# Performance work log

Measured on AMD Instinct MI355X. Metric: run time of the kernel, lower is better.

Reference implementation:

```python
import jax, jax.numpy as jnp
import numpy as np

BETA = 0.25


def setup_inputs() -> dict:
    key = jax.random.key(0)
    k1, k2, k3, k4 = jax.random.split(key, 4)
    B, D, T, H, W = 2, 256, 8, 32, 32
    K = 8192
    z = jax.random.normal(k1, (B, D, T, H, W), dtype=jnp.float32)
    # nn.init.normal_(embedding.weight, mean=0, std=emb_dim ** -0.5)
    emb_w = jax.random.normal(k2, (K, D), dtype=jnp.float32) * (D ** -0.5)
    # torch Linear default init ~ U(-1/sqrt(in), 1/sqrt(in)); scaled normal is fine for a reference
    w1 = jax.random.normal(k3, (D, D), dtype=jnp.float32) * (D ** -0.5)
    w2 = jax.random.normal(k4, (D, D), dtype=jnp.float32) * (D ** -0.5)
    return {"z": z, "emb_w": emb_w, "w1": w1, "w2": w2}


def reference(z, emb_w, w1, w2):
    B, D, T, H, W = z.shape
    K = emb_w.shape[0]
    # permute to channels-last and flatten: [B,T,H,W,D] -> [N,D]
    z_cl = jnp.transpose(z, (0, 2, 3, 4, 1))
    z_flat = z_cl.reshape(-1, D)
    N = z_flat.shape[0]
    # simvq: Linear -> GELU (exact) -> Linear, both bias-free
    quant_codebook = jax.nn.gelu(emb_w @ w1.T, approximate=False) @ w2.T  # [K, D]
    # pairwise squared L2 distances [N, K]
    d = (
        jnp.sum(z_flat ** 2, axis=1, keepdims=True)
        + jnp.sum(quant_codebook ** 2, axis=1)
        - 2.0 * (z_flat @ quant_codebook.T)
    )
    mean_distance = jnp.mean(d)
    idx = jnp.argmin(d, axis=1)  # [N]
    # gather == one-hot @ codebook
    z_q_flat = quant_codebook[idx]  # [N, D]
    z_q = z_q_flat.reshape(z_cl.shape)
    # VQ loss with stop-gradients
    loss = jnp.mean((jax.lax.stop_gradient(z_q) - z_cl) ** 2) + BETA * jnp.mean(
        (z_q - jax.lax.stop_gradient(z_cl)) ** 2
    )
    # straight-through estimator
    z_q = z_cl + jax.lax.stop_gradient(z_q - z_cl)
    # perplexity from code usage histogram (== mean of one-hot encodings)
    counts = jnp.zeros((K,), dtype=jnp.float32).at[idx].add(1.0)
    e_mean = counts / N
    perplexity = jnp.exp(-jnp.sum(e_mean * jnp.log(e_mean + 1e-10)))
    # back to channels-first [B, D, T, H, W]
    z_q = jnp.transpose(z_q, (0, 4, 1, 2, 3))
    return z_q, loss, perplexity, mean_distance
```

## Files before the change

### kernel.cpp

```cpp
#include <hip/hip_runtime.h>
#include <math.h>

#define BATCH 2
#define DIM   256
#define THW   8192
#define NTOK  16384
#define KCB   8192
#define OUTQ  4194304
#define CAP   2000000
#define SCAP  5600

typedef short short8 __attribute__((ext_vector_type(8)));
typedef float f32x4 __attribute__((ext_vector_type(4)));

__device__ __forceinline__ unsigned short f2bf_rn(float v) {
    unsigned u = __float_as_uint(v);
    unsigned r = u + 0x7FFFu + ((u >> 16) & 1u);
    return (unsigned short)(r >> 16);
}
__device__ __forceinline__ float bf2f(unsigned short b) {
    return __uint_as_float((unsigned)b << 16);
}
__device__ __forceinline__ void gl2lds16(const unsigned short* g, unsigned short* l) {
    __builtin_amdgcn_global_load_lds(
        (const __attribute__((address_space(1))) void*)g,
        (__attribute__((address_space(3))) void*)l, 16, 0, 0);
}

__global__ void k_splitW(const float* __restrict__ w1, const float* __restrict__ w2,
                         unsigned short* __restrict__ W1s, unsigned short* __restrict__ W2s,
                         int* __restrict__ counts,
                         unsigned* __restrict__ tileMaxC, unsigned* __restrict__ tileMaxCl,
                         float* __restrict__ accums,
                         float* __restrict__ partialZ, float* __restrict__ partialC) {
    int bid = blockIdx.x;
    int t = threadIdx.x;
    if (bid < 32) {
        counts[bid * 256 + t] = 0;
    } else if (bid == 32) {
        if (t < 64) { tileMaxC[t] = 0u; tileMaxCl[t] = 0u; }
        if (t >= 64 && t < 72) accums[t - 64] = 0.f;
    } else if (bid == 33) {
        partialZ[t] = 0.f;
    } else if (bid == 34) {
        partialC[t] = 0.f;
    }
    int row = bid & 255;
    const float* src = (bid >> 8) ? w2 : w1;
    unsigned short* dst = ((bid >> 8) ? W2s : W1s) + (size_t)row * 768;
    float v = src[row * 256 + t];
    unsigned short hb = f2bf_rn(v);
    unsigned short lb = f2bf_rn(v - bf2f(hb));
    dst[t] = hb;
    dst[256 + t] = hb;
    dst[512 + t] = lb;
}

__global__ void k_buildA(const float* __restrict__ z,
                         unsigned short* __restrict__ Ahi,
                         unsigned short* __restrict__ Alo,
                         float* __restrict__ zsq,
                         float* __restrict__ sA, float* __restrict__ sB,
                         float* __restrict__ partialZ,
                         unsigned long long* __restrict__ packed,
                         unsigned long long* __restrict__ packed2) {
    __shared__ ushort2 tile[64][65];
    __shared__ float zacc[64];
    __shared__ float lacc[64];
    __shared__ float pz[256];
    int t = threadIdx.x;
    int n0 = blockIdx.x * 64;
    int b = n0 >> 13;
    int thw0 = n0 & 8191;
    if (t < 64) {
        zacc[t] = 0.f; lacc[t] = 0.f;
        packed[n0 + t] = ~0ull;
        packed2[n0 + t] = ~0ull;
    }
    pz[t] = 0.f;
    __syncthreads();
    int nn_r = t & 63, dg = t >> 6;
    float a1 = 0.f, a2 = 0.f;
    for (int dc = 0; dc < 256; dc += 64) {
        for (int r = 0; r < 16; ++r) {
            int dd = r * 4 + dg;
            float v = z[((size_t)(b * 256 + dc + dd)) * 8192 + thw0 + nn_r];
            unsigned short hb = f2bf_rn(v);
            float hf = bf2f(hb);
            unsigned short lb = f2bf_rn(v - hf);
            float lf = bf2f(lb);
            tile[dd][nn_r] = make_ushort2(hb, lb);
            a1 += v * v;
            a2 += lf * lf;
        }
        __syncthreads();
        int kk = t & 63, ng = t >> 6;
        float dimsum = 0.f;
        for (int i2 = 0; i2 < 16; ++i2) {
            int nn = ng + i2 * 4;
            ushort2 hl = tile[kk][nn];
            size_t base = (size_t)(n0 + nn) * 256;
            Ahi[base + dc + kk] = hl.x;
            Alo[base + dc + kk] = hl.y;
            dimsum += bf2f(hl.x) + bf2f(hl.y);
        }
        atomicAdd(&pz[dc + kk], dimsum);
        __syncthreads();
    }
    atomicAdd(&zacc[nn_r], a1);
    atomicAdd(&lacc[nn_r], a2);
    __syncthreads();
    if (t < 64) {
        zsq[n0 + t] = zacc[t];
        sA[n0 + t] = 2.1f * sqrtf(lacc[t]);
        sB[n0 + t] = 2.1f * sqrtf(zacc[t]);
    }
    atomicAdd(&partialZ[t], pz[t]);
}

__global__ void k_buildE(const float* __restrict__ emb, unsigned short* __restrict__ E) {
    int t = threadIdx.x;
    int row = blockIdx.x * 4 + (t >> 6);
    int e4 = (t & 63) * 4;
    float4 v = *(const float4*)&emb[(size_t)row * 256 + e4];
    ushort4 hi, lo;
    hi.x = f2bf_rn(v.x); lo.x = f2bf_rn(v.x - bf2f(hi.x));
    hi.y = f2bf_rn(v.y); lo.y = f2bf_rn(v.y - bf2f(hi.y));
    hi.z = f2bf_rn(v.z); lo.z = f2bf_rn(v.z - bf2f(hi.z));
    hi.w = f2bf_rn(v.w); lo.w = f2bf_rn(v.w - bf2f(hi.w));
    size_t base = (size_t)row * 768;
    *(ushort4*)&E[base + e4] = hi;
    *(ushort4*)&E[base + 256 + e4] = lo;
    *(ushort4*)&E[base + 512 + e4] = hi;
}

template <int GELU>
__global__ __launch_bounds__(256) void k_mlp(const unsigned short* __restrict__ A,
                                             const unsigned short* __restrict__ B,
                                             unsigned short* __restrict__ Hs,
                                             float* __restrict__ C_t) {
    __shared__ __align__(16) char smem[32768];
    unsigned short* Asm = (unsigned short*)smem;
    unsigned short* Bsm = (unsigned short*)(smem + 16384);

    int t = threadIdx.x;
    int lane = t & 63;
    int w = t >> 6;
    int wm = w >> 1, wn = w & 1;
    int m0 = blockIdx.y * 128;
    int n0 = blockIdx.x * 128;

    int rA = w * 8 + (lane >> 3);
    int ch_l = lane & 7;
    int ch_g = ch_l ^ (lane >> 3);
    const unsigned short* gA = A + (size_t)(m0 + rA) * 768 + ch_g * 8;
    const unsigned short* gB = B + (size_t)(n0 + rA) * 768 + ch_g * 8;
    unsigned short* lA = &Asm[rA * 64 + ch_l * 8];
    unsigned short* lB = &Bsm[rA * 64 + ch_l * 8];

    f32x4 acc[4][4];
#pragma unroll
    for (int i = 0; i < 4; ++i)
#pragma unroll
        for (int j = 0; j < 4; ++j)
            acc[i][j] = f32x4{0.f, 0.f, 0.f, 0.f};

#pragma unroll
    for (int i = 0; i < 4; ++i) {
        gl2lds16(gA + (size_t)(32 * i) * 768, lA + 32 * i * 64);
        gl2lds16(gB + (size_t)(32 * i) * 768, lB + 32 * i * 64);
    }
    __syncthreads();

    int l15 = lane & 15;
    int quad = lane >> 4;
    int sw = l15 & 7;
    for (int kc = 0; kc < 12; ++kc) {
#pragma unroll
        for (int kk = 0; kk < 2; ++kk) {
            short8 a[4], b[4];
#pragma unroll
            for (int i = 0; i < 4; ++i)
                a[i] = *(const short8*)&Asm[(wm * 64 + i * 16 + l15) * 64 +
                                            (((kk * 4 + quad) ^ sw) * 8)];
#pragma unroll
            for (int j = 0; j < 4; ++j)
                b[j] = *(const short8*)&Bsm[(wn * 64 + j * 16 + l15) * 64 +
                                            (((kk * 4 + quad) ^ sw) * 8)];
#pragma unroll
            for (int i = 0; i < 4; ++i)
#pragma unroll
                for (int j = 0; j < 4; ++j)
                    acc[i][j] = __builtin_amdgcn_mfma_f32_16x16x32_bf16(a[i], b[j], acc[i][j], 0, 0, 0);
        }
        __syncthreads();
        if (kc < 11) {
            int ko = (kc + 1) * 64;
#pragma unroll
            for (int i = 0; i < 4; ++i) {
                gl2lds16(gA + (size_t)(32 * i) * 768 + ko, lA + 32 * i * 64);
                gl2lds16(gB + (size_t)(32 * i) * 768 + ko, lB + 32 * i * 64);
            }
            __syncthreads();
        }
    }

#pragma unroll
    for (int i = 0; i < 4; ++i) {
#pragma unroll
        for (int reg = 0; reg < 4; ++reg) {
            int mrow = m0 + wm * 64 + i * 16 + quad * 4 + reg;
#pragma unroll
            for (int j = 0; j < 4; ++j) {
                int ncol = n0 + wn * 64 + j * 16 + l15;
                float h = acc[i][j][reg];
                if (GELU) {
                    float g = 0.5f * h * (1.f + erff(h * 0.70710678118654752f));
                    unsigned short hb = f2bf_rn(g);
                    unsigned short lb = f2bf_rn(g - bf2f(hb));
                    size_t base = (size_t)mrow * 768;
                    Hs[base + ncol] = hb;
                    Hs[base + 256 + ncol] = lb;
                    Hs[base + 512 + ncol] = hb;
                } else {
                    C_t[(size_t)mrow * 8192 + ncol] = h;
                }
            }
        }
    }
}

__global__ void k_buildB(const float* __restrict__ C_t,
                         unsigned short* __restrict__ Bhi,
                         unsigned short* __restrict__ Blo,
                         float* __restrict__ csq,
                         float* __restrict__ sC, float* __restrict__ sCl,
                         unsigned* __restrict__ tileMaxC, unsigned* __restrict__ tileMaxCl,
                         float* __restrict__ accums, float* __restrict__ partialC) {
    __shared__ ushort2 tile[64][65];
    __shared__ float kacc[64];
    __shared__ float lacc[64];
    __shared__ float pc[256];
    int t = threadIdx.x;
    int k0 = blockIdx.x * 64;
    if (t < 64) { kacc[t] = 0.f; lacc[t] = 0.f; }
    pc[t] = 0.f;
    __syncthreads();
    int nn_r = t & 63, dg = t >> 6;
    float a1 = 0.f, a2 = 0.f;
    for (int dc = 0; dc < 256; dc += 64) {
        for (int r = 0; r < 16; ++r) {
            int dd = r * 4 + dg;
            float v = C_t[(size_t)(dc + dd) * KCB + k0 + nn_r];
            unsigned short hb = f2bf_rn(v);
            float hf = bf2f(hb);
            unsigned short lb = f2bf_rn(v - hf);
            float lf = bf2f(lb);
            tile[dd][nn_r] = make_ushort2(hb, lb);
            a1 += v * v;
            a2 += lf * lf;
        }
        __syncthreads();
        int kk = t & 63, ng = t >> 6;
        float dimsum = 0.f;
        for (int i2 = 0; i2 < 16; ++i2) {
            int nn = ng + i2 * 4;
            ushort2 hl = tile[kk][nn];
            size_t base = (size_t)(k0 + nn) * 256;
            Bhi[base + dc + kk] = hl.x;
            Blo[base + dc + kk] = hl.y;
            dimsum += bf2f(hl.x) + bf2f(hl.y);
        }
        atomicAdd(&pc[dc + kk], dimsum);
        __syncthreads();
    }
    atomicAdd(&kacc[nn_r], a1);
    atomicAdd(&lacc[nn_r], a2);
    __syncthreads();
    if (t < 64) {
        float c2 = kacc[t], l2 = lacc[t];
        float sc = sqrtf(c2), sl = sqrtf(l2);
        csq[k0 + t] = c2;
        sC[k0 + t] = sc;
        sCl[k0 + t] = sl;
        int tl = blockIdx.x >> 1;
        atomicMax(&tileMaxC[tl], __float_as_uint(sc));
        atomicMax(&tileMaxCl[tl], __float_as_uint(sl));
        atomicMax((unsigned*)&accums[3], __float_as_uint(c2));
        atomicMax((unsigned*)&accums[4], __float_as_uint(l2));
    }
    atomicAdd(&partialC[t], pc[t]);
}

__global__ __launch_bounds__(512, 2) void k_dist_hi(const unsigned short* __restrict__ A,
                                                    const unsigned short* __restrict__ B,
                                                    const float* __restrict__ zsq,
                                                    const float* __restrict__ csq,
                                                    const float* __restrict__ sA,
                                                    const float* __restrict__ sB,
                                                    const unsigned* __restrict__ tileMaxC,
                                                    const unsigned* __restrict__ tileMaxCl,
                                                    unsigned long long* __restrict__ packed,
                                                    float* __restrict__ accums,
                                                    unsigned long long* __restrict__ cand) {
    __shared__ __align__(16) char smem[131072];
    float* sbd     = (float*)smem;
    float* gprev_s = (float*)(smem + 2048);
    float* thr     = (float*)(smem + 3072);
    unsigned* scnt  = (unsigned*)(smem + 4096);
    unsigned* sbase = (unsigned*)(smem + 4100);
    unsigned long long* scand = (unsigned long long*)(smem + 4112);

    int t = threadIdx.x;
    int lane = t & 63;
    int w = t >> 6;
    int wm = w >> 1, wn = w & 1;
    int m0 = blockIdx.x * 256;
    int n0 = blockIdx.y * 256;

    int rA0 = w * 8 + (lane >> 3);
    int ch_l = lane & 7;
    int ch_g = ch_l ^ (lane >> 3);
    const unsigned short* gA = A + (size_t)(m0 + rA0) * 256 + ch_g * 8;
    const unsigned short* gB = B + (size_t)(n0 + rA0) * 256 + ch_g * 8;
    unsigned short* smemU = (unsigned short*)smem;
    unsigned short* lA = smemU + rA0 * 64 + ch_l * 8;
    unsigned short* lB = smemU + 16384 + rA0 * 64 + ch_l * 8;

    int l15 = lane & 15;
    int quad = lane >> 4;
    int sw = l15 & 7;

    float M1 = sqrtf(accums[3]);
    float M2 = sqrtf(accums[4]);
    float msC  = fmaxf(__uint_as_float(tileMaxC[2 * blockIdx.y]),
                       __uint_as_float(tileMaxC[2 * blockIdx.y + 1]));
    float msCl = fmaxf(__uint_as_float(tileMaxCl[2 * blockIdx.y]),
                       __uint_as_float(tileMaxCl[2 * blockIdx.y + 1]));
    float cv[8];
    int cols[8];
#pragma unroll
    for (int j = 0; j < 8; ++j) {
        int cloc = wn * 128 + j * 16 + l15;
        cols[j] = n0 + cloc;
        cv[j] = csq[cols[j]];
    }

    f32x4 acc[4][8];
#pragma unroll
    for (int i = 0; i < 4; ++i)
#pragma unroll
        for (int j = 0; j < 8; ++j)
            acc[i][j] = f32x4{0.f, 0.f, 0.f, 0.f};

#define STAGE(B_, KO)                                                       \
    {                                                                       \
        int off_ = (B_) * 32768;                                            \
        _Pragma("unroll")                                                   \
        for (int i_ = 0; i_ < 4; ++i_)                                      \
            gl2lds16(gA + (size_t)(64 * i_) * 256 + (KO),                   \
                     lA + off_ + 64 * i_ * 64);                             \
        _Pragma("unroll")                                                   \
        for (int i_ = 0; i_ < 4; ++i_)                                      \
            gl2lds16(gB + (size_t)(64 * i_) * 256 + (KO),                   \
                     lB + off_ + 64 * i_ * 64);                             \
    }

    STAGE(0, 0)
    __syncthreads();

    int cur = 0;
    for (int kc = 0; kc < 4; ++kc) {
        if (kc < 3) STAGE(cur ^ 1, (kc + 1) * 64)
        const unsigned short* Ar = smemU + cur * 32768;
        const unsigned short* Br = Ar + 16384;
#pragma unroll
        for (int kk = 0; kk < 2; ++kk) {
            short8 a[4], b[8];
#pragma unroll
            for (int i = 0; i < 4; ++i)
                a[i] = *(const short8*)&Ar[(wm * 64 + i * 16 + l15) * 64 +
                                            (((kk * 4 + quad) ^ sw) * 8)];
#pragma unroll
            for (int j = 0; j < 8; ++j)
                b[j] = *(const short8*)&Br[(wn * 128 + j * 16 + l15) * 64 +
                                            (((kk * 4 + quad) ^ sw) * 8)];
#pragma unroll
            for (int i = 0; i < 4; ++i)
#pragma unroll
                for (int j = 0; j < 8; ++j)
                    acc[i][j] = __builtin_amdgcn_mfma_f32_16x16x32_bf16(a[i], b[j], acc[i][j], 0, 0, 0);
        }
        __syncthreads();
        cur ^= 1;
    }
#undef STAGE

    if (t == 0) *scnt = 0;
    if (t < 256) {
        const unsigned* hp = (const unsigned*)&packed[m0 + t];
        gprev_s[t] = __uint_as_float(__atomic_load_n(hp + 1, __ATOMIC_RELAXED));
    }
#pragma unroll
    for (int i = 0; i < 4; ++i) {
#pragma unroll
        for (int reg = 0; reg < 4; ++reg) {
            int rloc = wm * 64 + i * 16 + quad * 4 + reg;
            float zs = zsq[m0 + rloc];
            float bd = 3.4e38f;
#pragma unroll
            for (int j = 0; j < 8; ++j) {
                float d = (zs + cv[j]) - 2.0f * acc[i][j][reg];
                acc[i][j][reg] = d;
                bd = fminf(bd, d);
            }
#pragma unroll
            for (int off = 1; off < 16; off <<= 1)
                bd = fminf(bd, __shfl_xor(bd, off, 64));
            if (l15 == 0) sbd[wn * 256 + rloc] = bd;
        }
    }
    __syncthreads();
    if (t < 256) {
        float bd = fminf(sbd[t], sbd[256 + t]);
        atomicMin(&packed[m0 + t], (unsigned long long)__float_as_uint(bd) << 32);
        float g = fminf(bd, gprev_s[t]);
        thr[t] = g + 1e-3f + sA[m0 + t] * (M1 + msC) + sB[m0 + t] * (M2 + msCl);
    }
    __syncthreads();
    unsigned* cnt = (unsigned*)&accums[2];
#pragma unroll
    for (int i = 0; i < 4; ++i) {
#pragma unroll
        for (int reg = 0; reg < 4; ++reg) {
            int rloc = wm * 64 + i * 16 + quad * 4 + reg;
            float tr = thr[rloc];
            bool p[8];
            bool any = false;
#pragma unroll
            for (int j = 0; j < 8; ++j) {
                p[j] = acc[i][j][reg] <= tr;
                any |= p[j];
            }
            if (__ballot(any)) {
                unsigned rbits = (unsigned)((m0 + rloc) << 13);
#pragma unroll
                for (int j = 0; j < 8; ++j) {
                    if (p[j]) {
                        unsigned long long entry =
                            ((unsigned long long)__float_as_uint(acc[i][j][reg]) << 32) |
                            (rbits | (unsigned)cols[j]);
                        unsigned pos = atomicAdd(scnt, 1u);
                        if (pos < SCAP) scand[pos] = entry;
                        else {
                            unsigned gp2 = atomicAdd(cnt, 1u);
                            if (gp2 < CAP) cand[gp2] = entry;
                        }
                    }
                }
            }
        }
    }
    __syncthreads();
    if (t == 0) {
        unsigned m = *scnt;
        if (m > SCAP) m = SCAP;
        *scnt = m;
        *sbase = atomicAdd(cnt, m);
    }
    __syncthreads();
    {
        unsigned m = *scnt, b0 = *sbase;
        for (unsigned u = t; u < m; u += 512)
            if (b0 + u < CAP) cand[b0 + u] = scand[u];
    }
}

__global__ __launch_bounds__(256) void k_rescore(const unsigned long long* __restrict__ cand,
                                                 const unsigned short* __restrict__ Ahi,
                                                 const unsigned short* __restrict__ Alo,
                                                 const unsigned short* __restrict__ Bhi,
                                                 const unsigned short* __restrict__ Blo,
                                                 const float* __restrict__ zsq,
                                                 const float* __restrict__ csq,
                                                 const float* __restrict__ sA,
                                                 const float* __restrict__ sB,
                                                 const float* __restrict__ sC,
                                                 const float* __restrict__ sCl,
                                                 const unsigned long long* __restrict__ packed,
                                                 unsigned long long* __restrict__ packed2,
                                                 const float* __restrict__ accums) {
    __shared__ unsigned long long q[256];
    __shared__ unsigned qn;
    unsigned total = *(const unsigned*)&accums[2];
    if (total > CAP) total = CAP;
    float M1 = sqrtf(accums[3]);
    float M2 = sqrtf(accums[4]);
    int t = threadIdx.x;
    int lane = t & 63;
    int w = t >> 6;
    unsigned per = (total + gridDim.x - 1) / gridDim.x;
    unsigned e0 = blockIdx.x * per;
    unsigned e1 = e0 + per;
    if (e1 > total) e1 = total;
    for (unsigned base = e0; base < e1; base += 256) {
        if (t == 0) qn = 0;
        __syncthreads();
        unsigned e = base + (unsigned)t;
        bool pass = false;
        unsigned long long ent = 0;
        if (e < e1) {
            ent = cand[e];
            float dhi = __uint_as_float((unsigned)(ent >> 32));
            unsigned nk = (unsigned)ent;
            int n = (nk >> 13) & 16383;
            int k = nk & 8191;
            float g = __uint_as_float((unsigned)(packed[n] >> 32));
            float marg = g + 1e-3f + sA[n] * (M1 + sC[k]) + sB[n] * (M2 + sCl[k]);
            pass = (dhi <= marg);
        }
        unsigned long long mask = __ballot(pass);
        if (mask) {
            unsigned cw = (unsigned)__popcll(mask);
            unsigned wbase = 0;
            if (lane == 0) wbase = atomicAdd(&qn, cw);
            wbase = __shfl(wbase, 0, 64);
            if (pass) {
                unsigned pos = wbase +
                    (unsigned)__popcll(mask & ((1ull << lane) - 1ull));
                q[pos] = ent;
            }
        }
        __syncthreads();
        unsigned m = qn;
        for (unsigned i = (unsigned)w; i < m; i += 4) {
            unsigned long long e2 = q[i];
            unsigned nk = (unsigned)e2;
            int n = (nk >> 13) & 16383;
            int k = nk & 8191;
            ushort4 zh = *((const ushort4*)(Ahi + (size_t)n * 256) + lane);
            ushort4 zl = *((const ushort4*)(Alo + (size_t)n * 256) + lane);
            ushort4 ch = *((const ushort4*)(Bhi + (size_t)k * 256) + lane);
            ushort4 cl = *((const ushort4*)(Blo + (size_t)k * 256) + lane);
            float s = (bf2f(zh.x) + bf2f(zl.x)) * (bf2f(ch.x) + bf2f(cl.x))
                    + (bf2f(zh.y) + bf2f(zl.y)) * (bf2f(ch.y) + bf2f(cl.y))
                    + (bf2f(zh.z) + bf2f(zl.z)) * (bf2f(ch.z) + bf2f(cl.z))
                    + (bf2f(zh.w) + bf2f(zl.w)) * (bf2f(ch.w) + bf2f(cl.w));
#pragma unroll
            for (int off = 1; off < 64; off <<= 1)
                s += __shfl_xor(s, off, 64);
            if (lane == 0) {
                float dd = (zsq[n] + csq[k]) - 2.0f * s;
                unsigned long long p =
                    ((unsigned long long)__float_as_uint(dd) << 32) | (unsigned)k;
                atomicMin(&packed2[n], p);
            }
        }
        __syncthreads();
    }
}

__global__ void k_zqloss(const float* __restrict__ z, const float* __restrict__ C_t,
                         const unsigned long long* __restrict__ packed2,
                         float* __restrict__ out, float* __restrict__ loss_sum,
                         int* __restrict__ counts) {
    __shared__ float red[256];
    int bid = blockIdx.x;
    int b = bid >> 8;
    int d = bid & 255;
    int t = threadIdx.x;
    if (t < 32) {
        int kk = (int)(unsigned)packed2[bid * 32 + t] & 8191;
        atomicAdd(&counts[kk], 1);
    }
    const float* crow = C_t + (size_t)d * KCB;
    const unsigned long long* pb = packed2 + (size_t)b * THW;
    size_t base = ((size_t)(b * DIM + d)) * THW;
    float lsum = 0.f;
    for (int it = 0; it < 8; ++it) {
        int thw = it * 1024 + t * 4;
        ulonglong2 p01 = *(const ulonglong2*)&pb[thw];
        ulonglong2 p23 = *(const ulonglong2*)&pb[thw + 2];
        int i0 = (int)(unsigned)p01.x & 8191;
        int i1 = (int)(unsigned)p01.y & 8191;
        int i2 = (int)(unsigned)p23.x & 8191;
        int i3 = (int)(unsigned)p23.y & 8191;
        float4 zz = *(const float4*)&z[base + thw];
        float4 v;
        v.x = crow[i0]; v.y = crow[i1]; v.z = crow[i2]; v.w = crow[i3];
        *(float4*)&out[base + thw] = v;
        float d0 = v.x - zz.x, d1 = v.y - zz.y, d2 = v.z - zz.z, d3 = v.w - zz.w;
        lsum += d0 * d0 + d1 * d1 + d2 * d2 + d3 * d3;
    }
    red[t] = lsum;
    __syncthreads();
    for (int s = 128; s > 0; s >>= 1) {
        if (t < s) red[t] += red[t + s];
        __syncthreads();
    }
    if (t == 0) atomicAdd(loss_sum, red[0]);
}

__global__ void k_scalars(const int* __restrict__ counts,
                          const float* __restrict__ accums,
                          const float* __restrict__ zsq, const float* __restrict__ csq,
                          const float* __restrict__ partialZ,
                          const float* __restrict__ partialC,
                          float* __restrict__ out_tail) {
    __shared__ double redd[256];
    __shared__ float redf[256];
    int t = threadIdx.x;
    double szsq = 0.0, scsq = 0.0;
    for (int n = t; n < NTOK; n += 256) szsq += (double)zsq[n];
    for (int k = t; k < KCB; k += 256) scsq += (double)csq[k];
    float SZ = partialZ[t];
    float SC = partialC[t];
    double total = 8192.0 * szsq + 16384.0 * scsq - 2.0 * (double)SZ * (double)SC;
    redd[t] = total;
    float s = 0.f;
    for (int k = t; k < KCB; k += 256) {
        float e = (float)counts[k] * (1.0f / 16384.0f);
        s += e * logf(e + 1e-10f);
    }
    redf[t] = s;
    __syncthreads();
    for (int st = 128; st > 0; st >>= 1) {
        if (t < st) { redd[t] += redd[t + st]; redf[t] += redf[t + st]; }
        __syncthreads();
    }
    if (t == 0) {
        out_tail[0] = 1.25f * accums[1] / 4194304.0f;
        out_tail[1] = expf(-redf[0]);
        out_tail[2] = (float)(redd[0] / (16384.0 * 8192.0));
    }
}

extern "C" void kernel_launch(void* const* d_in, const int* in_sizes, int n_in,
                              void* d_out, int out_size, void* d_ws, size_t ws_size,
                              hipStream_t stream) {
    const float* z     = (const float*)d_in[0];
    const float* emb_w = (const float*)d_in[1];
    const float* w1    = (const float*)d_in[2];
    const float* w2    = (const float*)d_in[3];
    float* out = (float*)d_out;

    char* w = (char*)d_ws;
    unsigned short* Ahi = (unsigned short*)(w + 0);
    unsigned short* Alo = (unsigned short*)(w + 8388608);
    unsigned short* Ebf = (unsigned short*)(w + 16777216);
    unsigned short* Bhi = (unsigned short*)(w + 29360128);
    unsigned short* Blo = (unsigned short*)(w + 33554432);
    unsigned short* W1s = (unsigned short*)(w + 37748736);
    unsigned short* W2s = (unsigned short*)(w + 38141952);
    float* zsq   = (float*)(w + 38535168);
    float* sA    = (float*)(w + 38666240);
    float* sB    = (float*)(w + 38731776);
    float* csq   = (float*)(w + 38797312);
    float* sC    = (float*)(w + 38862848);
    float* sCl   = (float*)(w + 38895616);
    unsigned long long* packed  = (unsigned long long*)(w + 38928384);
    unsigned long long* packed2 = (unsigned long long*)(w + 39059456);
    int*   counts = (int*)(w + 39256064);
    float* partialZ = (float*)(w + 39288832);
    float* partialC = (float*)(w + 39550976);
    unsigned* tileMaxC  = (unsigned*)(w + 39682048);
    unsigned* tileMaxCl = (unsigned*)(w + 39682304);
    float* accums = (float*)(w + 39682560);

    float* C_t = (float*)Ebf;
    unsigned short* Hs = (unsigned short*)d_out;
    unsigned long long* cand = (unsigned long long*)d_out;

    k_splitW<<<512, 256, 0, stream>>>(w1, w2, W1s, W2s, counts,
                                      tileMaxC, tileMaxCl, accums, partialZ, partialC);
    k_buildA<<<NTOK / 64, 256, 0, stream>>>(z, Ahi, Alo, zsq, sA, sB, partialZ,
                                            packed, packed2);
    k_buildE<<<KCB / 4, 256, 0, stream>>>(emb_w, Ebf);

    k_mlp<1><<<dim3(2, KCB / 128), 256, 0, stream>>>(Ebf, W1s, Hs, nullptr);
    k_mlp<0><<<dim3(KCB / 128, 2), 256, 0, stream>>>(W2s, Hs, nullptr, C_t);

    k_buildB<<<KCB / 64, 256, 0, stream>>>(C_t, Bhi, Blo, csq, sC, sCl,
                                           tileMaxC, tileMaxCl, accums, partialC);

    k_dist_hi<<<dim3(NTOK / 256, KCB / 256), 512, 0, stream>>>(
        Ahi, Bhi, zsq, csq, sA, sB, tileMaxC, tileMaxCl, packed, accums, cand);

    k_rescore<<<1024, 256, 0, stream>>>(cand, Ahi, Alo, Bhi, Blo, zsq, csq,
                                        sA, sB, sC, sCl, packed, packed2, accums);

    k_zqloss<<<BATCH * DIM, 256, 0, stream>>>(z, C_t, packed2, out, accums + 1, counts);
    k_scalars<<<1, 256, 0, stream>>>(counts, accums, zsq, csq, partialZ, partialC, out + OUTQ);
}
```

Measured before the change: 380.3 us.

## Merge prep kernels, double-buffer MLP GEMM with 64-row tiles, widen rescore grid

Combines the three preprocessing kernels (weight split, z conversion, embedding conversion) into one launch so block roles are chosen by block index, which saves two launches. The MLP GEMM now uses 64-row M tiles to double the number of blocks, and it double-buffers LDS so the next K chunk loads while the current one is being computed. The rescore grid is doubled. The cost is larger LDS use per block and a smaller per-wave tile, which lowers MFMA reuse.

```diff
diff --git a/kernel.cpp b/kernel.cpp
--- a/kernel.cpp
+++ b/kernel.cpp
@@ -27,49 +27,63 @@
         (__attribute__((address_space(3))) void*)l, 16, 0, 0);
 }
 
-__global__ void k_splitW(const float* __restrict__ w1, const float* __restrict__ w2,
-                         unsigned short* __restrict__ W1s, unsigned short* __restrict__ W2s,
-                         int* __restrict__ counts,
-                         unsigned* __restrict__ tileMaxC, unsigned* __restrict__ tileMaxCl,
-                         float* __restrict__ accums,
-                         float* __restrict__ partialZ, float* __restrict__ partialC) {
-    int bid = blockIdx.x;
-    int t = threadIdx.x;
-    if (bid < 32) {
-        counts[bid * 256 + t] = 0;
-    } else if (bid == 32) {
-        if (t < 64) { tileMaxC[t] = 0u; tileMaxCl[t] = 0u; }
-        if (t >= 64 && t < 72) accums[t - 64] = 0.f;
-    } else if (bid == 33) {
-        partialZ[t] = 0.f;
-    } else if (bid == 34) {
-        partialC[t] = 0.f;
-    }
-    int row = bid & 255;
-    const float* src = (bid >> 8) ? w2 : w1;
-    unsigned short* dst = ((bid >> 8) ? W2s : W1s) + (size_t)row * 768;
-    float v = src[row * 256 + t];
-    unsigned short hb = f2bf_rn(v);
-    unsigned short lb = f2bf_rn(v - bf2f(hb));
-    dst[t] = hb;
-    dst[256 + t] = hb;
-    dst[512 + t] = lb;
-}
-
-__global__ void k_buildA(const float* __restrict__ z,
-                         unsigned short* __restrict__ Ahi,
-                         unsigned short* __restrict__ Alo,
-                         float* __restrict__ zsq,
-                         float* __restrict__ sA, float* __restrict__ sB,
-                         float* __restrict__ partialZ,
-                         unsigned long long* __restrict__ packed,
-                         unsigned long long* __restrict__ packed2) {
+__global__ void k_prep(const float* __restrict__ w1, const float* __restrict__ w2,
+                       unsigned short* __restrict__ W1s, unsigned short* __restrict__ W2s,
+                       int* __restrict__ counts,
+                       unsigned* __restrict__ tileMaxC, unsigned* __restrict__ tileMaxCl,
+                       float* __restrict__ accums,
+                       float* __restrict__ partialZ, float* __restrict__ partialC,
+                       const float* __restrict__ z,
+                       unsigned short* __restrict__ Ahi, unsigned short* __restrict__ Alo,
+                       float* __restrict__ zsq, float* __restrict__ sA, float* __restrict__ sB,
+                       unsigned long long* __restrict__ packed,
+                       unsigned long long* __restrict__ packed2,
+                       const float* __restrict__ emb, unsigned short* __restrict__ E) {
     __shared__ ushort2 tile[64][65];
     __shared__ float zacc[64];
     __shared__ float lacc[64];
     __shared__ float pz[256];
+    int bid = blockIdx.x;
     int t = threadIdx.x;
-    int n0 = blockIdx.x * 64;
+
+    if (bid < 512) {
+        if (bid < 32) {
+            counts[bid * 256 + t] = 0;
+        } else if (bid == 32) {
+            if (t < 64) { tileMaxC[t] = 0u; tileMaxCl[t] = 0u; }
+            if (t >= 64 && t < 72) accums[t - 64] = 0.f;
+        } else if (bid == 33) {
+            partialZ[t] = 0.f;
+        } else if (bid == 34) {
+            partialC[t] = 0.f;
+        }
+        int row = bid & 255;
+        const float* src = (bid >> 8) ? w2 : w1;
+        unsigned short* dst = ((bid >> 8) ? W2s : W1s) + (size_t)row * 768;
+        float v = src[row * 256 + t];
+        unsigned short hb = f2bf_rn(v);
+        unsigned short lb = f2bf_rn(v - bf2f(hb));
+        dst[t] = hb;
+        dst[256 + t] = hb;
+        dst[512 + t] = lb;
+        return;
+    }
+    if (bid >= 768) {
+        int row = (bid - 768) * 4 + (t >> 6);
+        int e4 = (t & 63) * 4;
+        float4 v = *(const float4*)&emb[(size_t)row * 256 + e4];
+        ushort4 hi, lo;
+        hi.x = f2bf_rn(v.x); lo.x = f2bf_rn(v.x - bf2f(hi.x));
+        hi.y = f2bf_rn(v.y); lo.y = f2bf_rn(v.y - bf2f(hi.y));
+        hi.z = f2bf_rn(v.z); lo.z = f2bf_rn(v.z - bf2f(hi.z));
+        hi.w = f2bf_rn(v.w); lo.w = f2bf_rn(v.w - bf2f(hi.w));
+        size_t base = (size_t)row * 768;
+        *(ushort4*)&E[base + e4] = hi;
+        *(ushort4*)&E[base + 256 + e4] = lo;
+        *(ushort4*)&E[base + 512 + e4] = hi;
+        return;
+    }
+    int n0 = (bid - 512) * 64;
     int b = n0 >> 13;
     int thw0 = n0 & 8191;
     if (t < 64) {
@@ -118,98 +132,85 @@
     atomicAdd(&partialZ[t], pz[t]);
 }
 
-__global__ void k_buildE(const float* __restrict__ emb, unsigned short* __restrict__ E) {
-    int t = threadIdx.x;
-    int row = blockIdx.x * 4 + (t >> 6);
-    int e4 = (t & 63) * 4;
-    float4 v = *(const float4*)&emb[(size_t)row * 256 + e4];
-    ushort4 hi, lo;
-    hi.x = f2bf_rn(v.x); lo.x = f2bf_rn(v.x - bf2f(hi.x));
-    hi.y = f2bf_rn(v.y); lo.y = f2bf_rn(v.y - bf2f(hi.y));
-    hi.z = f2bf_rn(v.z); lo.z = f2bf_rn(v.z - bf2f(hi.z));
-    hi.w = f2bf_rn(v.w); lo.w = f2bf_rn(v.w - bf2f(hi.w));
-    size_t base = (size_t)row * 768;
-    *(ushort4*)&E[base + e4] = hi;
-    *(ushort4*)&E[base + 256 + e4] = lo;
-    *(ushort4*)&E[base + 512 + e4] = hi;
-}
-
 template <int GELU>
 __global__ __launch_bounds__(256) void k_mlp(const unsigned short* __restrict__ A,
                                              const unsigned short* __restrict__ B,
                                              unsigned short* __restrict__ Hs,
                                              float* __restrict__ C_t) {
-    __shared__ __align__(16) char smem[32768];
-    unsigned short* Asm = (unsigned short*)smem;
-    unsigned short* Bsm = (unsigned short*)(smem + 16384);
+    __shared__ __align__(16) char smem[49152];
+    unsigned short* smemU = (unsigned short*)smem;
 
     int t = threadIdx.x;
     int lane = t & 63;
     int w = t >> 6;
     int wm = w >> 1, wn = w & 1;
-    int m0 = blockIdx.y * 128;
+    int m0 = blockIdx.y * 64;
     int n0 = blockIdx.x * 128;
 
-    int rA = w * 8 + (lane >> 3);
+    int rA0 = w * 8 + (lane >> 3);
     int ch_l = lane & 7;
-    int ch_g = ch_l ^ (lane >> 3);
-    const unsigned short* gA = A + (size_t)(m0 + rA) * 768 + ch_g * 8;
-    const unsigned short* gB = B + (size_t)(n0 + rA) * 768 + ch_g * 8;
-    unsigned short* lA = &Asm[rA * 64 + ch_l * 8];
-    unsigned short* lB = &Bsm[rA * 64 + ch_l * 8];
-
-    f32x4 acc[4][4];
-#pragma unroll
-    for (int i = 0; i < 4; ++i)
+    int ch_g = ch_l ^ (rA0 & 7);
+    const unsigned short* gA = A + (size_t)(m0 + rA0) * 768 + ch_g * 8;
+    const unsigned short* gB = B + (size_t)(n0 + rA0) * 768 + ch_g * 8;
+    int lds0 = rA0 * 64 + ch_l * 8;
+
+    f32x4 acc[2][4];
+#pragma unroll
+    for (int i = 0; i < 2; ++i)
 #pragma unroll
         for (int j = 0; j < 4; ++j)
             acc[i][j] = f32x4{0.f, 0.f, 0.f, 0.f};
 
-#pragma unroll
-    for (int i = 0; i < 4; ++i) {
-        gl2lds16(gA + (size_t)(32 * i) * 768, lA + 32 * i * 64);
-        gl2lds16(gB + (size_t)(32 * i) * 768, lB + 32 * i * 64);
-    }
+#define MSTAGE(BUF, KO)                                                     \
+    {                                                                       \
+        unsigned short* ba_ = smemU + (BUF) * 12288;                        \
+        gl2lds16(gA + (KO), ba_ + lds0);                                    \
+        gl2lds16(gA + (KO) + (size_t)32 * 768, ba_ + 2048 + lds0);          \
+        _Pragma("unroll")                                                   \
+        for (int g_ = 0; g_ < 4; ++g_)                                      \
+            gl2lds16(gB + (KO) + (size_t)(32 * g_) * 768,                   \
+                     ba_ + 4096 + g_ * 2048 + lds0);                        \
+    }
+
+    MSTAGE(0, 0)
     __syncthreads();
 
     int l15 = lane & 15;
     int quad = lane >> 4;
     int sw = l15 & 7;
+    int cur = 0;
     for (int kc = 0; kc < 12; ++kc) {
+        if (kc < 11) MSTAGE(cur ^ 1, (kc + 1) * 64)
+        const unsigned short* Ar = smemU + cur * 12288;
+        const unsigned short* Br = Ar + 4096;
 #pragma unroll
         for (int kk = 0; kk < 2; ++kk) {
-            short8 a[4], b[4];
-#pragma unroll
-            for (int i = 0; i < 4; ++i)
-                a[i] = *(const short8*)&Asm[(wm * 64 + i * 16 + l15) * 64 +
-                                            (((kk * 4 + quad) ^ sw) * 8)];
+            short8 a[2], b[4];
+#pragma unroll
+            for (int i = 0; i < 2; ++i)
+                a[i] = *(const short8*)&Ar[(wm * 32 + i * 16 + l15) * 64 +
+                                           (((kk * 4 + quad) ^ sw) * 8)];
 #pragma unroll
             for (int j = 0; j < 4; ++j)
-                b[j] = *(const short8*)&Bsm[(wn * 64 + j * 16 + l15) * 64 +
-                                            (((kk * 4 + quad) ^ sw) * 8)];
-#pragma unroll
-            for (int i = 0; i < 4; ++i)
+                b[j] = *(const short8*)&Br[(wn * 64 + j * 16 + l15) * 64 +
+                                           (((kk * 4 + quad) ^ sw) * 8)];
+#pragma unroll
+            for (int i = 0; i < 2; ++i)
 #pragma unroll
                 for (int j = 0; j < 4; ++j)
-                    acc[i][j] = __builtin_amdgcn_mfma_f32_16x16x32_bf16(a[i], b[j], acc[i][j], 0, 0, 0);
-        }
-        __syncthreads();
-        if (kc < 11) {
-            int ko = (kc + 1) * 64;
-#pragma unroll
-            for (int i = 0; i < 4; ++i) {
-                gl2lds16(gA + (size_t)(32 * i) * 768 + ko, lA + 32 * i * 64);
-                gl2lds16(gB + (size_t)(32 * i) * 768 + ko, lB + 32 * i * 64);
-            }
-            __syncthreads();
-        }
-    }
-
-#pragma unroll
-    for (int i = 0; i < 4; ++i) {
+                    acc[i][j] = __builtin_amdgcn_mfma_f32_16x16x32_bf16(
+                        a[i], b[j], acc[i][j], 0, 0, 0);
+        }
+        __syncthreads();
+        cur ^= 1;
+    }
+#undef MSTAGE
+
+#pragma unroll
+    for (int i = 0; i < 2; ++i) {
 #pragma unroll
         for (int reg = 0; reg < 4; ++reg) {
-            int mrow = m0 + wm * 64 + i * 16 + quad * 4 + reg;
+            int mrow = m0 + wm * 32 + i * 16 + quad * 4 + reg;
 #pragma unroll
             for (int j = 0; j < 4; ++j) {
                 int ncol = n0 + wn * 64 + j * 16 + l15;
@@ -671,14 +672,13 @@
     unsigned short* Hs = (unsigned short*)d_out;
     unsigned long long* cand = (unsigned long long*)d_out;
 
-    k_splitW<<<512, 256, 0, stream>>>(w1, w2, W1s, W2s, counts,
-                                      tileMaxC, tileMaxCl, accums, partialZ, partialC);
-    k_buildA<<<NTOK / 64, 256, 0, stream>>>(z, Ahi, Alo, zsq, sA, sB, partialZ,
-                                            packed, packed2);
-    k_buildE<<<KCB / 4, 256, 0, stream>>>(emb_w, Ebf);
-
-    k_mlp<1><<<dim3(2, KCB / 128), 256, 0, stream>>>(Ebf, W1s, Hs, nullptr);
-    k_mlp<0><<<dim3(KCB / 128, 2), 256, 0, stream>>>(W2s, Hs, nullptr, C_t);
+    k_prep<<<2816, 256, 0, stream>>>(w1, w2, W1s, W2s, counts,
+                                     tileMaxC, tileMaxCl, accums, partialZ, partialC,
+                                     z, Ahi, Alo, zsq, sA, sB, packed, packed2,
+                                     emb_w, Ebf);
+
+    k_mlp<1><<<dim3(2, 128), 256, 0, stream>>>(Ebf, W1s, Hs, nullptr);
+    k_mlp<0><<<dim3(64, 4), 256, 0, stream>>>(W2s, Hs, nullptr, C_t);
 
     k_buildB<<<KCB / 64, 256, 0, stream>>>(C_t, Bhi, Blo, csq, sC, sCl,
                                            tileMaxC, tileMaxCl, accums, partialC);
@@ -686,7 +686,7 @@
     k_dist_hi<<<dim3(NTOK / 256, KCB / 256), 512, 0, stream>>>(
         Ahi, Bhi, zsq, csq, sA, sB, tileMaxC, tileMaxCl, packed, accums, cand);
 
-    k_rescore<<<1024, 256, 0, stream>>>(cand, Ahi, Alo, Bhi, Blo, zsq, csq,
+    k_rescore<<<2048, 256, 0, stream>>>(cand, Ahi, Alo, Bhi, Blo, zsq, csq,
                                         sA, sB, sC, sCl, packed, packed2, accums);
 
     k_zqloss<<<BATCH * DIM, 256, 0, stream>>>(z, C_t, packed2, out, accums + 1, counts);
```

New measurement: 355.7 us. -6.5%, faster.
